# Kernel optimization log

Hardware: AMD Instinct MI355X
Metric: run time of the kernel (lower is better)

## Reference

```python
import jax, jax.numpy as jnp
import numpy as np

NEG_SLOPE = 0.2  # PyG GATConv default negative_slope


def _entity_embedding(r_emb, attr_emb, femb_w, femb_b):
    # r_emb: [N, Dr], attr_emb: [N, A, Da]; femb: Linear(Da->De)
    rp = r_emb @ femb_w.T + femb_b                      # [N, De]
    ap = attr_emb @ femb_w.T + femb_b                   # [N, A, De]
    scores = jnp.einsum('nd,nad->na', rp, ap)           # [N, A]
    att = jax.nn.softmax(scores, axis=1)
    return jnp.einsum('na,nad->nd', att, ap)            # [N, De]


def _gat_conv(x, edge_index, w, a_src, a_dst, bias):
    # Single-head GATConv (PyG defaults: add_self_loops=True, negative_slope=0.2)
    n = x.shape[0]
    loop = jnp.arange(n, dtype=edge_index.dtype)
    src = jnp.concatenate([edge_index[0], loop])
    dst = jnp.concatenate([edge_index[1], loop])
    h = x @ w.T                                         # [N, Do]
    alpha_s = h @ a_src                                 # [N]
    alpha_d = h @ a_dst                                 # [N]
    e = jax.nn.leaky_relu(alpha_s[src] + alpha_d[dst], NEG_SLOPE)  # [E+N]
    m = jax.ops.segment_max(e, dst, num_segments=n)
    ex = jnp.exp(e - m[dst])
    denom = jax.ops.segment_sum(ex, dst, num_segments=n)
    alpha = ex / denom[dst]
    out = jax.ops.segment_sum(alpha[:, None] * h[src], dst, num_segments=n)
    return out + bias


def setup_inputs() -> dict:
    key = jax.random.key(0)
    ks = jax.random.split(key, 16)
    N, A, E = 50000, 16, 800000
    NUM_ATTR, NUM_REL = 50000, 500
    Da = De = Dr = 128
    Din1 = De + Dr  # gat1 input dim
    inp = {
        'h_attributes': jax.random.randint(ks[0], (N, A), 0, NUM_ATTR),
        't_attributes': jax.random.randint(ks[1], (N, A), 0, NUM_ATTR),
        'r_idx': jax.random.randint(ks[2], (N,), 0, NUM_REL),
        'edge_index': jax.random.randint(ks[3], (2, E), 0, N),
        'attr_table': jax.random.normal(ks[4], (NUM_ATTR, Da), jnp.float32),
        'rel_table': jax.random.normal(ks[5], (NUM_REL, Dr), jnp.float32),
        'femb_w': jax.random.normal(ks[6], (De, Da), jnp.float32) / np.sqrt(Da),
        'femb_b': jnp.zeros((De,), jnp.float32),
        'gat1_w': jax.random.normal(ks[7], (De, Din1), jnp.float32) / np.sqrt(Din1),
        'gat1_asrc': jax.random.normal(ks[8], (De,), jnp.float32) / np.sqrt(De),
        'gat1_adst': jax.random.normal(ks[9], (De,), jnp.float32) / np.sqrt(De),
        'gat1_b': jnp.zeros((De,), jnp.float32),
        'gat2_w': jax.random.normal(ks[10], (De, De), jnp.float32) / np.sqrt(De),
        'gat2_asrc': jax.random.normal(ks[11], (De,), jnp.float32) / np.sqrt(De),
        'gat2_adst': jax.random.normal(ks[12], (De,), jnp.float32) / np.sqrt(De),
        'gat2_b': jnp.zeros((De,), jnp.float32),
    }
    return inp


def reference(h_attributes, t_attributes, r_idx, edge_index,
              attr_table, rel_table, femb_w, femb_b,
              gat1_w, gat1_asrc, gat1_adst, gat1_b,
              gat2_w, gat2_asrc, gat2_adst, gat2_b):
    h_attr_emb = attr_table[h_attributes]               # [N, A, Da]
    t_attr_emb = attr_table[t_attributes]               # [N, A, Da]
    r_emb = rel_table[r_idx]                            # [N, Dr]
    h_emb = _entity_embedding(r_emb, h_attr_emb, femb_w, femb_b)  # [N, De]
    t_emb = _entity_embedding(r_emb, t_attr_emb, femb_w, femb_b)  # [N, De]
    # aggregate head/tail then concat relation -> [N, De + Dr] (matches gat1 in_dim)
    triple_emb = jnp.concatenate([h_emb + t_emb, r_emb], axis=1)
    x = _gat_conv(triple_emb, edge_index, gat1_w, gat1_asrc, gat1_adst, gat1_b)
    return _gat_conv(x, edge_index, gat2_w, gat2_asrc, gat2_adst, gat2_b)
```

## Files before the change

### kernel.cpp

```cpp
#include <hip/hip_runtime.h>
#include <math.h>

#define DE 128
#define NEG_SLOPE 0.2f
#define LOG2E 1.4426950408889634f
#define ESHIFT2 57.707801635559926f
#define ESHIFT_AGG 28.853900817779268f
#define EXP2(x) __builtin_amdgcn_exp2f(x)

typedef __attribute__((ext_vector_type(4))) float f4;
typedef __attribute__((ext_vector_type(2))) float f2;
typedef _Float16 half_t;
typedef __attribute__((ext_vector_type(2))) _Float16 h2;
typedef __attribute__((ext_vector_type(4))) _Float16 h4v;
typedef __attribute__((ext_vector_type(8))) _Float16 h8;

__device__ __forceinline__ float wave_red_bcast(float x) {
    union fi { float f; int i; };
    fi a; a.f = x;
    fi t;
    t.i = __builtin_amdgcn_update_dpp(0, a.i, 0x111, 0xf, 0xf, true); a.f += t.f;
    t.i = __builtin_amdgcn_update_dpp(0, a.i, 0x112, 0xf, 0xf, true); a.f += t.f;
    t.i = __builtin_amdgcn_update_dpp(0, a.i, 0x114, 0xf, 0xf, true); a.f += t.f;
    t.i = __builtin_amdgcn_update_dpp(0, a.i, 0x118, 0xf, 0xf, true); a.f += t.f;
    t.i = __builtin_amdgcn_update_dpp(0, a.i, 0x142, 0xa, 0xf, true); a.f += t.f;
    t.i = __builtin_amdgcn_update_dpp(0, a.i, 0x143, 0xc, 0xf, true); a.f += t.f;
    fi r; r.i = __builtin_amdgcn_readlane(a.i, 63);
    return r.f;
}

__device__ __forceinline__ float row16_allred(float x) {
    union fi { float f; int i; };
    fi a; a.f = x;
    fi t;
    t.i = __builtin_amdgcn_update_dpp(0, a.i, 0x121, 0xf, 0xf, true); a.f += t.f;
    t.i = __builtin_amdgcn_update_dpp(0, a.i, 0x122, 0xf, 0xf, true); a.f += t.f;
    t.i = __builtin_amdgcn_update_dpp(0, a.i, 0x124, 0xf, 0xf, true); a.f += t.f;
    t.i = __builtin_amdgcn_update_dpp(0, a.i, 0x128, 0xf, 0xf, true); a.f += t.f;
    return a.f;
}

__global__ __launch_bounds__(256) void k_count(const int* __restrict__ ei, int E, int N,
                                               int* __restrict__ cnt) {
    int e = blockIdx.x * blockDim.x + threadIdx.x;
    int total = E + N;
    if (e >= total) return;
    int dst = (e < E) ? ei[E + e] : (e - E);
    atomicAdd(&cnt[dst], 1);
}

__global__ __launch_bounds__(1024) void k_scan(const int* __restrict__ cnt, int n,
                                               int* __restrict__ indptr) {
    __shared__ int wsum[16];
    __shared__ int btot;
    int tid = threadIdx.x, lane = tid & 63, w = tid >> 6;
    int carry = 0;
    for (int base = 0; base < n; base += 1024) {
        int i = base + tid;
        int v = (i < n) ? cnt[i] : 0;
        int x = v;
#pragma unroll
        for (int off = 1; off < 64; off <<= 1) {
            int t = __shfl_up(x, off, 64);
            if (lane >= off) x += t;
        }
        if (lane == 63) wsum[w] = x;
        __syncthreads();
        if (w == 0) {
            int s = (lane < 16) ? wsum[lane] : 0;
#pragma unroll
            for (int off = 1; off < 16; off <<= 1) {
                int t = __shfl_up(s, off, 64);
                if (lane >= off) s += t;
            }
            if (lane < 16) wsum[lane] = s;
            if (lane == 15) btot = s;
        }
        __syncthreads();
        int wexcl = (w == 0) ? 0 : wsum[w - 1];
        if (i < n) indptr[i] = carry + wexcl + (x - v);
        carry += btot;
        __syncthreads();
    }
    if (tid == 0) indptr[n] = carry;
}

__global__ __launch_bounds__(256) void k_fill(const int* __restrict__ ei, int E, int N,
                                              const int* __restrict__ indptr,
                                              int* __restrict__ cur, int* __restrict__ adj) {
    int e = blockIdx.x * blockDim.x + threadIdx.x;
    int total = E + N;
    if (e >= total) return;
    int src, dst;
    if (e < E) { src = ei[e]; dst = ei[E + e]; }
    else       { src = dst = e - E; }
    int pos = indptr[dst] + atomicAdd(&cur[dst], 1);
    adj[pos] = src;
}

__global__ __launch_bounds__(256) void k_gemm_rel(const float* __restrict__ in, int rows,
                                                  const float* __restrict__ W1,
                                                  const float* __restrict__ bias1,
                                                  float* __restrict__ out1,
                                                  const float* __restrict__ W2,
                                                  float* __restrict__ out2) {
    const float* W; int ldw, wcol0; const float* bias; float* out;
    if (blockIdx.y == 0) { W = W1; ldw = DE;     wcol0 = 0;  bias = bias1;   out = out1; }
    else                 { W = W2; ldw = 2 * DE; wcol0 = DE; bias = nullptr; out = out2; }

    __shared__ float Wt[128 * 128];
    const int tid = threadIdx.x;
#pragma unroll
    for (int it = 0; it < 16; ++it) {
        int idx = it * 256 + tid;
        int c = idx & 127, k4 = idx >> 7;
        f4 wv = *(const f4*)(W + (size_t)c * ldw + wcol0 + k4 * 4);
#pragma unroll
        for (int j = 0; j < 4; ++j) Wt[(4 * k4 + j) * 128 + c] = wv[j];
    }
    __syncthreads();

    const int RPT = 2;
    const int cgrp = tid & 15, rgrp = tid >> 4;
    const int c0 = cgrp * 4;
    const int row0 = blockIdx.x * (16 * RPT) + rgrp * RPT;

    const float* rowp[RPT];
#pragma unroll
    for (int i = 0; i < RPT; ++i)
        rowp[i] = in + (size_t)min(row0 + i, rows - 1) * 128;

    float acc[RPT][8];
#pragma unroll
    for (int i = 0; i < RPT; ++i)
#pragma unroll
        for (int j = 0; j < 8; ++j) acc[i][j] = 0.f;

#pragma unroll 1
    for (int k = 0; k < 128; k += 4) {
        f4 a[RPT];
#pragma unroll
        for (int i = 0; i < RPT; ++i) a[i] = *(const f4*)(rowp[i] + k);
#pragma unroll
        for (int kk = 0; kk < 4; ++kk) {
            f4 b0 = *(const f4*)&Wt[(k + kk) * 128 + c0];
            f4 b1 = *(const f4*)&Wt[(k + kk) * 128 + c0 + 64];
#pragma unroll
            for (int i = 0; i < RPT; ++i) {
                float av = a[i][kk];
#pragma unroll
                for (int j = 0; j < 4; ++j) {
                    acc[i][j]     = fmaf(av, b0[j], acc[i][j]);
                    acc[i][j + 4] = fmaf(av, b1[j], acc[i][j + 4]);
                }
            }
        }
    }
    f4 bi0 = {0.f,0.f,0.f,0.f}, bi1 = {0.f,0.f,0.f,0.f};
    if (bias) { bi0 = *(const f4*)(bias + c0); bi1 = *(const f4*)(bias + c0 + 64); }
#pragma unroll
    for (int i = 0; i < RPT; ++i) {
        int r = row0 + i;
        if (r < rows) {
            f4 v0, v1;
#pragma unroll
            for (int j = 0; j < 4; ++j) { v0[j] = acc[i][j] + bi0[j]; v1[j] = acc[i][j+4] + bi1[j]; }
            *(f4*)(out + (size_t)r * 128 + c0) = v0;
            *(f4*)(out + (size_t)r * 128 + c0 + 64) = v1;
        }
    }
}

template <typename AT>
__global__ __launch_bounds__(256) void k_gemm_mfma(const AT* __restrict__ A, int rows,
                                                   const float* __restrict__ W, int ldw, int wcol0,
                                                   const float* __restrict__ bias,
                                                   const float* __restrict__ addtab,
                                                   const int* __restrict__ addidx,
                                                   const float* __restrict__ avs,
                                                   const float* __restrict__ avd,
                                                   float* __restrict__ als,
                                                   float* __restrict__ ald,
                                                   half_t* __restrict__ out16) {
    __shared__ alignas(16) char ldsbuf[128 * 136 * 2];
    half_t* Wl = (half_t*)ldsbuf;
    float*  Dl = (float*)ldsbuf;

    const int tid = threadIdx.x;
    const int row0 = blockIdx.x * 64;

    for (int i = tid * 4; i < 128 * 128; i += 1024) {
        int c = i >> 7, k = i & 127;
        f4 wv = *(const f4*)(W + (size_t)c * ldw + wcol0 + k);
        h4v hv = {(half_t)wv[0], (half_t)wv[1], (half_t)wv[2], (half_t)wv[3]};
        *(h4v*)(Wl + c * 136 + k) = hv;
    }
    __syncthreads();

    const int wv_id = tid >> 6, l = tid & 63, lr = l & 15, lk = l >> 4;
    const int r_a = min(row0 + wv_id * 16 + lr, rows - 1);

    h8 af[4];
#pragma unroll
    for (int ks = 0; ks < 4; ++ks) {
        if constexpr (sizeof(AT) == 4) {
            f4 a0 = *(const f4*)(A + (size_t)r_a * 128 + ks * 32 + lk * 8);
            f4 a1 = *(const f4*)(A + (size_t)r_a * 128 + ks * 32 + lk * 8 + 4);
            h8 v = {(half_t)a0[0], (half_t)a0[1], (half_t)a0[2], (half_t)a0[3],
                    (half_t)a1[0], (half_t)a1[1], (half_t)a1[2], (half_t)a1[3]};
            af[ks] = v;
        } else {
            af[ks] = *(const h8*)(A + (size_t)r_a * 128 + ks * 32 + lk * 8);
        }
    }

    f4 acc[8];
#pragma unroll
    for (int t = 0; t < 8; ++t) acc[t] = (f4){0.f, 0.f, 0.f, 0.f};
#pragma unroll
    for (int ks = 0; ks < 4; ++ks) {
#pragma unroll
        for (int t = 0; t < 8; ++t) {
            h8 bf = *(const h8*)(Wl + (t * 16 + lr) * 136 + ks * 32 + lk * 8);
            acc[t] = __builtin_amdgcn_mfma_f32_16x16x32_f16(af[ks], bf, acc[t], 0, 0, 0);
        }
    }
    __syncthreads();

#pragma unroll
    for (int t = 0; t < 8; ++t)
#pragma unroll
        for (int q = 0; q < 4; ++q)
            Dl[(wv_id * 16 + lk * 4 + q) * 132 + t * 16 + lr] = acc[t][q];
    __syncthreads();

    const int cl = (tid & 15) * 8;
    f4 bi0 = {0.f,0.f,0.f,0.f}, bi1 = bi0;
    if (bias) { bi0 = *(const f4*)(bias + cl); bi1 = *(const f4*)(bias + cl + 4); }
    f4 as0 = {0.f,0.f,0.f,0.f}, as1 = as0, ad0 = as0, ad1 = as0;
    if (als) {
        as0 = *(const f4*)(avs + cl) * LOG2E; as1 = *(const f4*)(avs + cl + 4) * LOG2E;
        ad0 = *(const f4*)(avd + cl) * LOG2E; ad1 = *(const f4*)(avd + cl + 4) * LOG2E;
    }
#pragma unroll
    for (int pass = 0; pass < 4; ++pass) {
        int lrow = pass * 16 + (tid >> 4);
        int r = row0 + lrow;
        bool ok = r < rows;
        f4 v0 = *(const f4*)(Dl + lrow * 132 + cl);
        f4 v1 = *(const f4*)(Dl + lrow * 132 + cl + 4);
        v0 += bi0; v1 += bi1;
        if (addtab) {
            int ri = addidx[min(r, rows - 1)];
            v0 += *(const f4*)(addtab + (size_t)ri * 128 + cl);
            v1 += *(const f4*)(addtab + (size_t)ri * 128 + cl + 4);
        }
        if (als) {
            float ps = 0.f, pd = 0.f;
#pragma unroll
            for (int j = 0; j < 4; ++j) {
                ps += v0[j] * as0[j] + v1[j] * as1[j];
                pd += v0[j] * ad0[j] + v1[j] * ad1[j];
            }
            ps = row16_allred(ps);
            pd = row16_allred(pd);
            if ((tid & 15) == 0 && ok) { als[r] = ps; ald[r] = pd; }
        }
        if (ok) {
            h8 o = {(half_t)v0[0], (half_t)v0[1], (half_t)v0[2], (half_t)v0[3],
                    (half_t)v1[0], (half_t)v1[1], (half_t)v1[2], (half_t)v1[3]};
            *(h8*)(out16 + (size_t)r * 128 + cl) = o;
        }
    }
}

__global__ __launch_bounds__(256) void k_entity(const int* __restrict__ hA,
                                                const int* __restrict__ tA,
                                                const int* __restrict__ ridx,
                                                const half_t* __restrict__ pattr,
                                                const float* __restrict__ prel,
                                                half_t* __restrict__ s_emb16, int N) {
    int w = (blockIdx.x * blockDim.x + threadIdx.x) >> 6;
    if (w >= N) return;
    w = __builtin_amdgcn_readfirstlane(w);
    const int lane = threadIdx.x & 63;
    const int c = lane * 2;
    const int ri = ridx[w];
    const f2 rp = *(const f2*)(prel + (size_t)ri * 128 + c);
    const h2 rph = {(half_t)(rp[0] * LOG2E), (half_t)(rp[1] * LOG2E)};
    const float init = (lane == 0) ? -ESHIFT2 : 0.f;
    const int* __restrict__ hp = hA + (size_t)w * 16;
    const int* __restrict__ tp = tA + (size_t)w * 16;
    const char* __restrict__ pb = (const char*)pattr;
    const unsigned cb = (unsigned)lane << 2;

    f2 oh = {0.f, 0.f}, ot = {0.f, 0.f};
    float sh = 0.f, st = 0.f;

    auto ld = [&](int idx) -> h2 {
        return *(const h2*)(pb + (((unsigned)idx << 8) + cb));
    };

    h2 bh[2][4], bt[2][4];
#pragma unroll
    for (int q = 0; q < 4; ++q) {
        bh[0][q] = ld(hp[q]);
        bt[0][q] = ld(tp[q]);
    }
#pragma unroll
    for (int b = 0; b < 4; ++b) {
        const int cur = b & 1, nxt = cur ^ 1;
        if (b < 3) {
#pragma unroll
            for (int q = 0; q < 4; ++q) {
                bh[nxt][q] = ld(hp[4 * (b + 1) + q]);
                bt[nxt][q] = ld(tp[4 * (b + 1) + q]);
            }
        }
        float pph[4], ppt[4];
#pragma unroll
        for (int q = 0; q < 4; ++q) {
            pph[q] = __builtin_amdgcn_fdot2(rph, bh[cur][q], init, false);
            ppt[q] = __builtin_amdgcn_fdot2(rph, bt[cur][q], init, false);
        }
        float Sh[4], St[4];
#pragma unroll
        for (int q = 0; q < 4; ++q) {
            Sh[q] = wave_red_bcast(pph[q]);
            St[q] = wave_red_bcast(ppt[q]);
        }
#pragma unroll
        for (int q = 0; q < 4; ++q) {
            float wh = EXP2(Sh[q]);
            float wt = EXP2(St[q]);
            sh += wh; st += wt;
            oh[0] = fmaf(wh, (float)bh[cur][q][0], oh[0]);
            oh[1] = fmaf(wh, (float)bh[cur][q][1], oh[1]);
            ot[0] = fmaf(wt, (float)bt[cur][q][0], ot[0]);
            ot[1] = fmaf(wt, (float)bt[cur][q][1], ot[1]);
        }
    }
    float invh = 1.f / sh, invt = 1.f / st;
    h2 hv = {(half_t)(oh[0] * invh + ot[0] * invt),
             (half_t)(oh[1] * invh + ot[1] * invt)};
    *(h2*)(s_emb16 + (size_t)w * 128 + c) = hv;
}

__global__ __launch_bounds__(256) void k_aggregate(const int* __restrict__ indptr,
                                                   const int* __restrict__ adj,
                                                   const half_t* __restrict__ hsrc,
                                                   const float* __restrict__ als,
                                                   const float* __restrict__ ald,
                                                   const float* __restrict__ bias,
                                                   float* __restrict__ out,
                                                   half_t* __restrict__ out16, int N) {
    const int tid = threadIdx.x;
    const int wv = (blockIdx.x * 256 + tid) >> 6;
    const int nodeA = wv * 2;
    if (nodeA >= N) return;
    const int lane = tid & 63;
    const int node = min(nodeA + (lane >> 5), N - 1);
    const int sl = lane & 31;
    const int c = sl * 4;

    const int beg = indptr[node];
    const int deg = indptr[node + 1] - beg;
    const float adn = ald[node];
    const char* __restrict__ hb = (const char*)hsrc;
    const unsigned cb = (unsigned)sl << 3;

    float acc[4] = {0.f, 0.f, 0.f, 0.f};
    float exsum = 0.f;

    int cur[8], nxt[8];
#pragma unroll
    for (int q = 0; q < 8; ++q) cur[q] = adj[beg + q];

#pragma unroll 1
    for (int j0 = 0; j0 < deg; j0 += 8) {
        if (j0 + 8 < deg) {
#pragma unroll
            for (int q = 0; q < 8; ++q) nxt[q] = adj[beg + j0 + 8 + q];
        }
        int ss[8];
        float alv[8];
        h4v hv[8];
#pragma unroll
        for (int q = 0; q < 8; ++q)
            ss[q] = ((unsigned)cur[q] < (unsigned)N) ? cur[q] : 0;
#pragma unroll
        for (int q = 0; q < 8; ++q) alv[q] = als[ss[q]];
#pragma unroll
        for (int q = 0; q < 8; ++q)
            hv[q] = *(const h4v*)(hb + (((unsigned)ss[q] << 8) + cb));
#pragma unroll
        for (int q = 0; q < 8; ++q) {
            bool ok = (j0 + q) < deg;
            float e = alv[q] + adn;
            e = fmaxf(e, NEG_SLOPE * e);
            float ex = ok ? EXP2(e - ESHIFT_AGG) : 0.f;
            exsum += ex;
#pragma unroll
            for (int j = 0; j < 4; ++j) acc[j] = fmaf(ex, (float)hv[q][j], acc[j]);
        }
#pragma unroll
        for (int q = 0; q < 8; ++q) cur[q] = nxt[q];
    }

    float inv = 1.f / exsum;
    if (out) {
        f4 o;
#pragma unroll
        for (int j = 0; j < 4; ++j) o[j] = fmaf(acc[j], inv, bias[c + j]);
        *(f4*)(out + (size_t)node * 128 + c) = o;
    } else {
        h4v o;
#pragma unroll
        for (int j = 0; j < 4; ++j) o[j] = (half_t)fmaf(acc[j], inv, bias[c + j]);
        *(h4v*)(out16 + (size_t)node * 128 + c) = o;
    }
}

extern "C" void kernel_launch(void* const* d_in, const int* in_sizes, int n_in,
                              void* d_out, int out_size, void* d_ws, size_t ws_size,
                              hipStream_t stream) {
    const int*   hA   = (const int*)d_in[0];
    const int*   tA   = (const int*)d_in[1];
    const int*   rix  = (const int*)d_in[2];
    const int*   ei   = (const int*)d_in[3];
    const float* attr_table = (const float*)d_in[4];
    const float* rel_table  = (const float*)d_in[5];
    const float* femb_w = (const float*)d_in[6];
    const float* femb_b = (const float*)d_in[7];
    const float* g1w  = (const float*)d_in[8];
    const float* g1as = (const float*)d_in[9];
    const float* g1ad = (const float*)d_in[10];
    const float* g1b  = (const float*)d_in[11];
    const float* g2w  = (const float*)d_in[12];
    const float* g2as = (const float*)d_in[13];
    const float* g2ad = (const float*)d_in[14];
    const float* g2b  = (const float*)d_in[15];

    const int N  = in_sizes[2];
    const int E  = in_sizes[3] / 2;
    const int NA = in_sizes[4] / DE;
    const int NR = in_sizes[5] / DE;
    const int EN = E + N;

    char* p = (char*)d_ws;
    auto alloc = [&](size_t bytes) -> char* {
        char* q = p;
        p += (bytes + 255) & ~(size_t)255;
        return q;
    };
    half_t* proj16 = (half_t*)alloc((size_t)NA * DE * 2);
    half_t* s16    = (half_t*)alloc((size_t)N * DE * 2);
    half_t* h16    = (half_t*)alloc((size_t)N * DE * 2);
    half_t* x116   = (half_t*)alloc((size_t)N * DE * 2);
    float* prel    = (float*)alloc((size_t)NR * DE * 4);
    float* rel2    = (float*)alloc((size_t)NR * DE * 4);
    float* alps    = (float*)alloc((size_t)N * 4);
    float* alpd    = (float*)alloc((size_t)N * 4);
    int*   indptr  = (int*)alloc((size_t)(N + 1) * 4);
    int*   cnt     = (int*)alloc((size_t)N * 4);
    int*   cur     = (int*)alloc((size_t)N * 4);
    int*   adj     = (int*)alloc((size_t)(EN + 16) * 4);

    dim3 b256(256);

    hipMemsetAsync(cnt, 0, (size_t)((char*)cur - (char*)cnt) + (size_t)N * 4, stream);
    k_count<<<dim3((EN + 255) / 256), b256, 0, stream>>>(ei, E, N, cnt);
    k_scan<<<dim3(1), dim3(1024), 0, stream>>>(cnt, N, indptr);
    k_fill<<<dim3((EN + 255) / 256), b256, 0, stream>>>(ei, E, N, indptr, cur, adj);

    k_gemm_rel<<<dim3((NR + 31) / 32, 2), b256, 0, stream>>>(rel_table, NR,
        femb_w, femb_b, prel, g1w, rel2);

    k_gemm_mfma<float><<<dim3((NA + 63) / 64), b256, 0, stream>>>(attr_table, NA,
        femb_w, DE, 0, femb_b, nullptr, nullptr, nullptr, nullptr, nullptr, nullptr, proj16);

    k_entity<<<dim3((N + 3) / 4), b256, 0, stream>>>(hA, tA, rix, proj16, prel, s16, N);

    k_gemm_mfma<half_t><<<dim3((N + 63) / 64), b256, 0, stream>>>(s16, N,
        g1w, 2 * DE, 0, nullptr, rel2, rix, g1as, g1ad, alps, alpd, h16);
    k_aggregate<<<dim3((N + 7) / 8), b256, 0, stream>>>(indptr, adj, h16, alps, alpd, g1b,
                                                        nullptr, x116, N);

    k_gemm_mfma<half_t><<<dim3((N + 63) / 64), b256, 0, stream>>>(x116, N,
        g2w, DE, 0, nullptr, nullptr, nullptr, g2as, g2ad, alps, alpd, h16);
    k_aggregate<<<dim3((N + 7) / 8), b256, 0, stream>>>(indptr, adj, h16, alps, alpd, g2b,
                                                        (float*)d_out, nullptr, N);
}
```

Baseline: 305.0 us.

## Horizontally fuse independent preprocessing kernels and vectorize the CSR scan

Independent kernels are merged into shared launches that pick their work by block index: edge counting with the attribute-table GEMM, the relation GEMMs with the prefix scan, and CSR fill with entity embedding. This cuts the preprocessing launches from six to three and lets the single-block scan and the small relation GEMM run alongside other work. The scan is also rewritten for 256 threads, each loading four counts as an int4, with a simpler serial combine of the per-wave totals. In exchange, lightweight count and fill blocks now carry the larger shared-memory and register footprint of the kernels they are fused with, which can lower their occupancy.

```diff
diff --git a/kernel.cpp b/kernel.cpp
--- a/kernel.cpp
+++ b/kernel.cpp
@@ -40,25 +40,32 @@
     return a.f;
 }
 
-__global__ __launch_bounds__(256) void k_count(const int* __restrict__ ei, int E, int N,
-                                               int* __restrict__ cnt) {
-    int e = blockIdx.x * blockDim.x + threadIdx.x;
+__device__ __forceinline__ void count_body(int bid, const int* __restrict__ ei, int E, int N,
+                                           int* __restrict__ cnt) {
+    int e = bid * 256 + threadIdx.x;
     int total = E + N;
     if (e >= total) return;
     int dst = (e < E) ? ei[E + e] : (e - E);
     atomicAdd(&cnt[dst], 1);
 }
 
-__global__ __launch_bounds__(1024) void k_scan(const int* __restrict__ cnt, int n,
-                                               int* __restrict__ indptr) {
-    __shared__ int wsum[16];
-    __shared__ int btot;
-    int tid = threadIdx.x, lane = tid & 63, w = tid >> 6;
+__device__ void scan_body(const int* __restrict__ cnt, int n, int* __restrict__ indptr,
+                          char* smem) {
+    int* wsum = (int*)smem;
+    int* btot = (int*)smem + 4;
+    const int tid = threadIdx.x, lane = tid & 63, w = tid >> 6;
     int carry = 0;
     for (int base = 0; base < n; base += 1024) {
-        int i = base + tid;
-        int v = (i < n) ? cnt[i] : 0;
-        int x = v;
+        int i0 = base + tid * 4;
+        int4 v = {0, 0, 0, 0};
+        if (i0 + 3 < n) v = *(const int4*)(cnt + i0);
+        else {
+            if (i0 < n)     v.x = cnt[i0];
+            if (i0 + 1 < n) v.y = cnt[i0 + 1];
+            if (i0 + 2 < n) v.z = cnt[i0 + 2];
+        }
+        int s = v.x + v.y + v.z + v.w;
+        int x = s;
 #pragma unroll
         for (int off = 1; off < 64; off <<= 1) {
             int t = __shfl_up(x, off, 64);
@@ -66,29 +73,28 @@
         }
         if (lane == 63) wsum[w] = x;
         __syncthreads();
-        if (w == 0) {
-            int s = (lane < 16) ? wsum[lane] : 0;
-#pragma unroll
-            for (int off = 1; off < 16; off <<= 1) {
-                int t = __shfl_up(s, off, 64);
-                if (lane >= off) s += t;
-            }
-            if (lane < 16) wsum[lane] = s;
-            if (lane == 15) btot = s;
+        if (tid == 0) {
+            int acc = 0;
+#pragma unroll
+            for (int k = 0; k < 4; ++k) { int t = wsum[k]; wsum[k] = acc; acc += t; }
+            *btot = acc;
         }
         __syncthreads();
-        int wexcl = (w == 0) ? 0 : wsum[w - 1];
-        if (i < n) indptr[i] = carry + wexcl + (x - v);
-        carry += btot;
+        int excl = carry + wsum[w] + (x - s);
+        if (i0 < n)     indptr[i0]     = excl;
+        if (i0 + 1 < n) indptr[i0 + 1] = excl + v.x;
+        if (i0 + 2 < n) indptr[i0 + 2] = excl + v.x + v.y;
+        if (i0 + 3 < n) indptr[i0 + 3] = excl + v.x + v.y + v.z;
+        carry += *btot;
         __syncthreads();
     }
     if (tid == 0) indptr[n] = carry;
 }
 
-__global__ __launch_bounds__(256) void k_fill(const int* __restrict__ ei, int E, int N,
-                                              const int* __restrict__ indptr,
-                                              int* __restrict__ cur, int* __restrict__ adj) {
-    int e = blockIdx.x * blockDim.x + threadIdx.x;
+__device__ __forceinline__ void fill_body(int bid, const int* __restrict__ ei, int E, int N,
+                                          const int* __restrict__ indptr,
+                                          int* __restrict__ cur, int* __restrict__ adj) {
+    int e = bid * 256 + threadIdx.x;
     int total = E + N;
     if (e >= total) return;
     int src, dst;
@@ -98,17 +104,15 @@
     adj[pos] = src;
 }
 
-__global__ __launch_bounds__(256) void k_gemm_rel(const float* __restrict__ in, int rows,
-                                                  const float* __restrict__ W1,
-                                                  const float* __restrict__ bias1,
-                                                  float* __restrict__ out1,
-                                                  const float* __restrict__ W2,
-                                                  float* __restrict__ out2) {
+__device__ void rel_body(int bx, int sel, const float* __restrict__ in, int rows,
+                         const float* __restrict__ W1, const float* __restrict__ bias1,
+                         float* __restrict__ out1, const float* __restrict__ W2,
+                         float* __restrict__ out2, char* smem) {
     const float* W; int ldw, wcol0; const float* bias; float* out;
-    if (blockIdx.y == 0) { W = W1; ldw = DE;     wcol0 = 0;  bias = bias1;   out = out1; }
-    else                 { W = W2; ldw = 2 * DE; wcol0 = DE; bias = nullptr; out = out2; }
-
-    __shared__ float Wt[128 * 128];
+    if (sel == 0) { W = W1; ldw = DE;     wcol0 = 0;  bias = bias1;   out = out1; }
+    else          { W = W2; ldw = 2 * DE; wcol0 = DE; bias = nullptr; out = out2; }
+
+    float* Wt = (float*)smem;
     const int tid = threadIdx.x;
 #pragma unroll
     for (int it = 0; it < 16; ++it) {
@@ -123,7 +127,7 @@
     const int RPT = 2;
     const int cgrp = tid & 15, rgrp = tid >> 4;
     const int c0 = cgrp * 4;
-    const int row0 = blockIdx.x * (16 * RPT) + rgrp * RPT;
+    const int row0 = bx * (16 * RPT) + rgrp * RPT;
 
     const float* rowp[RPT];
 #pragma unroll
@@ -172,22 +176,21 @@
 }
 
 template <typename AT>
-__global__ __launch_bounds__(256) void k_gemm_mfma(const AT* __restrict__ A, int rows,
-                                                   const float* __restrict__ W, int ldw, int wcol0,
-                                                   const float* __restrict__ bias,
-                                                   const float* __restrict__ addtab,
-                                                   const int* __restrict__ addidx,
-                                                   const float* __restrict__ avs,
-                                                   const float* __restrict__ avd,
-                                                   float* __restrict__ als,
-                                                   float* __restrict__ ald,
-                                                   half_t* __restrict__ out16) {
-    __shared__ alignas(16) char ldsbuf[128 * 136 * 2];
-    half_t* Wl = (half_t*)ldsbuf;
-    float*  Dl = (float*)ldsbuf;
+__device__ void gemm_mfma_body(int bid, const AT* __restrict__ A, int rows,
+                               const float* __restrict__ W, int ldw, int wcol0,
+                               const float* __restrict__ bias,
+                               const float* __restrict__ addtab,
+                               const int* __restrict__ addidx,
+                               const float* __restrict__ avs,
+                               const float* __restrict__ avd,
+                               float* __restrict__ als,
+                               float* __restrict__ ald,
+                               half_t* __restrict__ out16, char* smem) {
+    half_t* Wl = (half_t*)smem;
+    float*  Dl = (float*)smem;
 
     const int tid = threadIdx.x;
-    const int row0 = blockIdx.x * 64;
+    const int row0 = bid * 64;
 
     for (int i = tid * 4; i < 128 * 128; i += 1024) {
         int c = i >> 7, k = i & 127;
@@ -274,13 +277,13 @@
     }
 }
 
-__global__ __launch_bounds__(256) void k_entity(const int* __restrict__ hA,
-                                                const int* __restrict__ tA,
-                                                const int* __restrict__ ridx,
-                                                const half_t* __restrict__ pattr,
-                                                const float* __restrict__ prel,
-                                                half_t* __restrict__ s_emb16, int N) {
-    int w = (blockIdx.x * blockDim.x + threadIdx.x) >> 6;
+__device__ void entity_body(int bid, const int* __restrict__ hA,
+                            const int* __restrict__ tA,
+                            const int* __restrict__ ridx,
+                            const half_t* __restrict__ pattr,
+                            const float* __restrict__ prel,
+                            half_t* __restrict__ s_emb16, int N) {
+    int w = (bid * 256 + (int)threadIdx.x) >> 6;
     if (w >= N) return;
     w = __builtin_amdgcn_readfirstlane(w);
     const int lane = threadIdx.x & 63;
@@ -344,6 +347,63 @@
     h2 hv = {(half_t)(oh[0] * invh + ot[0] * invt),
              (half_t)(oh[1] * invh + ot[1] * invt)};
     *(h2*)(s_emb16 + (size_t)w * 128 + c) = hv;
+}
+
+__global__ __launch_bounds__(256) void k_count_attr(const int* __restrict__ ei, int E, int N,
+                                                    int* __restrict__ cnt, int CB,
+                                                    const float* __restrict__ attr, int NA,
+                                                    const float* __restrict__ W,
+                                                    const float* __restrict__ bias,
+                                                    half_t* __restrict__ out16) {
+    __shared__ alignas(16) char smem[128 * 136 * 2];
+    int b = blockIdx.x;
+    if (b < CB) count_body(b, ei, E, N, cnt);
+    else gemm_mfma_body<float>(b - CB, attr, NA, W, DE, 0, bias, nullptr, nullptr,
+                               nullptr, nullptr, nullptr, nullptr, out16, smem);
+}
+
+__global__ __launch_bounds__(256) void k_rel_scan(const float* __restrict__ in, int rows,
+                                                  const float* __restrict__ W1,
+                                                  const float* __restrict__ b1,
+                                                  float* __restrict__ out1,
+                                                  const float* __restrict__ W2,
+                                                  float* __restrict__ out2, int RB,
+                                                  const int* __restrict__ cnt, int n,
+                                                  int* __restrict__ indptr) {
+    __shared__ alignas(16) char smem[128 * 128 * 4];
+    int b = blockIdx.x;
+    if (b < 2 * RB) rel_body(b % RB, b / RB, in, rows, W1, b1, out1, W2, out2, smem);
+    else scan_body(cnt, n, indptr, smem);
+}
+
+__global__ __launch_bounds__(256) void k_fill_entity(const int* __restrict__ ei, int E,
+                                                     const int* __restrict__ indptr,
+                                                     int* __restrict__ cur,
+                                                     int* __restrict__ adj, int FB,
+                                                     const int* __restrict__ hA,
+                                                     const int* __restrict__ tA,
+                                                     const int* __restrict__ ridx,
+                                                     const half_t* __restrict__ pattr,
+                                                     const float* __restrict__ prel,
+                                                     half_t* __restrict__ s_emb16, int N) {
+    int b = blockIdx.x;
+    if (b < FB) fill_body(b, ei, E, N, indptr, cur, adj);
+    else entity_body(b - FB, hA, tA, ridx, pattr, prel, s_emb16, N);
+}
+
+__global__ __launch_bounds__(256) void k_gemm_mfma_h(const half_t* __restrict__ A, int rows,
+                                                     const float* __restrict__ W, int ldw, int wcol0,
+                                                     const float* __restrict__ bias,
+                                                     const float* __restrict__ addtab,
+                                                     const int* __restrict__ addidx,
+                                                     const float* __restrict__ avs,
+                                                     const float* __restrict__ avd,
+                                                     float* __restrict__ als,
+                                                     float* __restrict__ ald,
+                                                     half_t* __restrict__ out16) {
+    __shared__ alignas(16) char smem[128 * 136 * 2];
+    gemm_mfma_body<half_t>(blockIdx.x, A, rows, W, ldw, wcol0, bias, addtab, addidx,
+                           avs, avd, als, ald, out16, smem);
 }
 
 __global__ __launch_bounds__(256) void k_aggregate(const int* __restrict__ indptr,
@@ -467,26 +527,29 @@
     int*   adj     = (int*)alloc((size_t)(EN + 16) * 4);
 
     dim3 b256(256);
+    const int CB = (EN + 255) / 256;
+    const int MB = (NA + 63) / 64;
+    const int RB = (NR + 31) / 32;
+    const int FB = CB;
+    const int EB = (N + 3) / 4;
 
     hipMemsetAsync(cnt, 0, (size_t)((char*)cur - (char*)cnt) + (size_t)N * 4, stream);
-    k_count<<<dim3((EN + 255) / 256), b256, 0, stream>>>(ei, E, N, cnt);
-    k_scan<<<dim3(1), dim3(1024), 0, stream>>>(cnt, N, indptr);
-    k_fill<<<dim3((EN + 255) / 256), b256, 0, stream>>>(ei, E, N, indptr, cur, adj);
-
-    k_gemm_rel<<<dim3((NR + 31) / 32, 2), b256, 0, stream>>>(rel_table, NR,
-        femb_w, femb_b, prel, g1w, rel2);
-
-    k_gemm_mfma<float><<<dim3((NA + 63) / 64), b256, 0, stream>>>(attr_table, NA,
-        femb_w, DE, 0, femb_b, nullptr, nullptr, nullptr, nullptr, nullptr, nullptr, proj16);
-
-    k_entity<<<dim3((N + 3) / 4), b256, 0, stream>>>(hA, tA, rix, proj16, prel, s16, N);
-
-    k_gemm_mfma<half_t><<<dim3((N + 63) / 64), b256, 0, stream>>>(s16, N,
+
+    k_count_attr<<<dim3(CB + MB), b256, 0, stream>>>(ei, E, N, cnt, CB,
+                                                     attr_table, NA, femb_w, femb_b, proj16);
+
+    k_rel_scan<<<dim3(2 * RB + 1), b256, 0, stream>>>(rel_table, NR, femb_w, femb_b, prel,
+                                                      g1w, rel2, RB, cnt, N, indptr);
+
+    k_fill_entity<<<dim3(FB + EB), b256, 0, stream>>>(ei, E, indptr, cur, adj, FB,
+                                                      hA, tA, rix, proj16, prel, s16, N);
+
+    k_gemm_mfma_h<<<dim3((N + 63) / 64), b256, 0, stream>>>(s16, N,
         g1w, 2 * DE, 0, nullptr, rel2, rix, g1as, g1ad, alps, alpd, h16);
     k_aggregate<<<dim3((N + 7) / 8), b256, 0, stream>>>(indptr, adj, h16, alps, alpd, g1b,
                                                         nullptr, x116, N);
 
-    k_gemm_mfma<half_t><<<dim3((N + 63) / 64), b256, 0, stream>>>(x116, N,
+    k_gemm_mfma_h<<<dim3((N + 63) / 64), b256, 0, stream>>>(x116, N,
         g2w, DE, 0, nullptr, nullptr, nullptr, g2as, g2ad, alps, alpd, h16);
     k_aggregate<<<dim3((N + 7) / 8), b256, 0, stream>>>(indptr, adj, h16, alps, alpd, g2b,
                                                         (float*)d_out, nullptr, N);
```

After: 293.0 us. 1.04x faster.
